# Kernel optimization log

Hardware: AMD Instinct MI355X
Metric: run time of the kernel (lower is better)

## Reference

```python
import jax, jax.numpy as jnp
import numpy as np

DIM = 1024
HEADS = 16
HIDDEN = 4 * DIM


def layernorm(x, g, b, eps=1e-5):
    mu = jnp.mean(x, axis=-1, keepdims=True)
    var = jnp.mean(jnp.square(x - mu), axis=-1, keepdims=True)
    return (x - mu) * jax.lax.rsqrt(var + eps) * g + b


def setup_inputs() -> dict:
    key = jax.random.key(0)
    ks = jax.random.split(key, 8)
    s = DIM ** -0.5
    return {
        "x": jax.random.normal(ks[0], (2, 2048, DIM), dtype=jnp.float32),
        "ln1_g": jnp.ones((DIM,), jnp.float32),
        "ln1_b": jnp.zeros((DIM,), jnp.float32),
        "qkv_w": jax.random.normal(ks[1], (DIM, 3 * DIM), jnp.float32) * s,
        "proj_w": jax.random.normal(ks[2], (DIM, DIM), jnp.float32) * s,
        "proj_b": jnp.zeros((DIM,), jnp.float32),
        "ln2_g": jnp.ones((DIM,), jnp.float32),
        "ln2_b": jnp.zeros((DIM,), jnp.float32),
        "fc1_w": jax.random.normal(ks[3], (DIM, HIDDEN), jnp.float32) * s,
        "fc1_b": jnp.zeros((HIDDEN,), jnp.float32),
        "fc2_w": jax.random.normal(ks[4], (HIDDEN, DIM), jnp.float32) * (HIDDEN ** -0.5),
        "fc2_b": jnp.zeros((DIM,), jnp.float32),
    }


def block_fwd(x, ln1_g, ln1_b, qkv_w, proj_w, proj_b, ln2_g, ln2_b,
              fc1_w, fc1_b, fc2_w, fc2_b):
    B, N, C = x.shape
    H = HEADS
    Dh = C // H
    scale = Dh ** -0.5
    # --- attention branch (pre-norm) ---
    h = layernorm(x, ln1_g, ln1_b)
    qkv = h @ qkv_w                     # [B,N,3C] (no bias: qkv_bias=False)
    qkv = qkv.reshape(B, N, 3, H, Dh)
    q = qkv[:, :, 0].transpose(0, 2, 1, 3)   # [B,H,N,Dh]
    k = qkv[:, :, 1].transpose(0, 2, 1, 3)
    v = qkv[:, :, 2].transpose(0, 2, 1, 3)
    attn = jnp.einsum('bhqd,bhkd->bhqk', q, k) * scale
    attn = jax.nn.softmax(attn, axis=-1)
    o = jnp.einsum('bhqk,bhkd->bhqd', attn, v)
    o = o.transpose(0, 2, 1, 3).reshape(B, N, C)
    x = x + (o @ proj_w + proj_b)
    # --- MLP branch (pre-norm) ---
    h = layernorm(x, ln2_g, ln2_b)
    h = jax.nn.gelu(h @ fc1_w + fc1_b, approximate=False)  # torch nn.GELU = exact erf
    x = x + (h @ fc2_w + fc2_b)
    return x


def reference(x, ln1_g, ln1_b, qkv_w, proj_w, proj_b, ln2_g, ln2_b,
              fc1_w, fc1_b, fc2_w, fc2_b):
    return block_fwd(x, ln1_g, ln1_b, qkv_w, proj_w, proj_b, ln2_g, ln2_b,
                     fc1_w, fc1_b, fc2_w, fc2_b)
```

## Files before the change

### kernel.cpp

```cpp
#include <hip/hip_runtime.h>
#include <math.h>

typedef unsigned short u16;
typedef unsigned int u32;
typedef __attribute__((ext_vector_type(8))) short short8;
typedef __attribute__((ext_vector_type(4))) float f32x4;
typedef __attribute__((ext_vector_type(2))) u32 u32x2;
typedef __attribute__((ext_vector_type(4))) u32 u32x4;
typedef __attribute__((ext_vector_type(4))) u16 u16x4;

typedef __attribute__((address_space(1))) const void gmem_t;
typedef __attribute__((address_space(3))) void lmem_t;

__device__ __forceinline__ u16 f2bf(float f) {
  u32 u = __builtin_bit_cast(u32, f);
  u = u + 0x7fffu + ((u >> 16) & 1u);
  return (u16)(u >> 16);
}

__device__ __forceinline__ u32 cvt_pk_bf16(float a, float b) {
  u32 r;
  asm("v_cvt_pk_bf16_f32 %0, %1, %2" : "=v"(r) : "v"(a), "v"(b));
  return r;
}

__device__ __forceinline__ void g2l16(const void* g, void* l) {
  __builtin_amdgcn_global_load_lds((gmem_t*)g, (lmem_t*)l, 16, 0, 0);
}

template <int N> __device__ __forceinline__ void waitcnt_vm() {
  if constexpr (N == 0)      asm volatile("s_waitcnt vmcnt(0)" ::: "memory");
  else if constexpr (N == 4) asm volatile("s_waitcnt vmcnt(4)" ::: "memory");
  else if constexpr (N == 6) asm volatile("s_waitcnt vmcnt(6)" ::: "memory");
  else if constexpr (N == 8) asm volatile("s_waitcnt vmcnt(8)" ::: "memory");
  else static_assert(N == 0 || N == 4 || N == 6 || N == 8, "add literal");
}

__global__ __launch_bounds__(256) void wtrans(const float* __restrict__ in,
                                              u16* __restrict__ out, int R, int C) {
  __shared__ float t[64][65];
  int tid = threadIdx.x;
  int nbx = C >> 6;
  int bx = blockIdx.x % nbx, by = blockIdx.x / nbx;
  int r0 = by << 6, c0 = bx << 6;
  int lr = tid >> 2, lc = (tid & 3) << 4;
  const float* src = in + (size_t)(r0 + lr) * C + c0 + lc;
#pragma unroll
  for (int j = 0; j < 4; ++j) {
    f32x4 v = *(const f32x4*)(src + j * 4);
    t[lr][lc + j * 4 + 0] = v.x; t[lr][lc + j * 4 + 1] = v.y;
    t[lr][lc + j * 4 + 2] = v.z; t[lr][lc + j * 4 + 3] = v.w;
  }
  __syncthreads();
  int oc = tid >> 2, orr = (tid & 3) << 4;
  u16* dst = out + (size_t)(c0 + oc) * R + r0 + orr;
  u32 u[8];
#pragma unroll
  for (int j = 0; j < 8; ++j)
    u[j] = (u32)f2bf(t[orr + 2 * j][oc]) | ((u32)f2bf(t[orr + 2 * j + 1][oc]) << 16);
  u32x4 v0; v0.x = u[0]; v0.y = u[1]; v0.z = u[2]; v0.w = u[3];
  u32x4 v1; v1.x = u[4]; v1.y = u[5]; v1.z = u[6]; v1.w = u[7];
  *(u32x4*)(dst) = v0;
  *(u32x4*)(dst + 8) = v1;
}

__global__ __launch_bounds__(256) void lnorm(const float* __restrict__ in,
                                             const float* __restrict__ gw,
                                             const float* __restrict__ bw,
                                             u16* __restrict__ out) {
  int r = blockIdx.x, tid = threadIdx.x;
  const f32x4 v = *((const f32x4*)(in + (size_t)r * 1024) + tid);
  float s = v.x + v.y + v.z + v.w;
  float ss = v.x * v.x + v.y * v.y + v.z * v.z + v.w * v.w;
#pragma unroll
  for (int o = 32; o >= 1; o >>= 1) { s += __shfl_xor(s, o); ss += __shfl_xor(ss, o); }
  __shared__ float red[8];
  int w = tid >> 6;
  if ((tid & 63) == 0) { red[w] = s; red[4 + w] = ss; }
  __syncthreads();
  s = red[0] + red[1] + red[2] + red[3];
  ss = red[4] + red[5] + red[6] + red[7];
  float mu = s * (1.0f / 1024.0f);
  float var = ss * (1.0f / 1024.0f) - mu * mu;
  float rstd = rsqrtf(var + 1e-5f);
  const f32x4 g4 = *((const f32x4*)gw + tid);
  const f32x4 b4 = *((const f32x4*)bw + tid);
  u16x4 o;
  o.x = f2bf((v.x - mu) * rstd * g4.x + b4.x);
  o.y = f2bf((v.y - mu) * rstd * g4.y + b4.y);
  o.z = f2bf((v.z - mu) * rstd * g4.z + b4.z);
  o.w = f2bf((v.w - mu) * rstd * g4.w + b4.w);
  *((u16x4*)(out + (size_t)r * 1024) + tid) = o;
}

template <int EPI, int BM, int BN>
__global__ __launch_bounds__(256, 2) void gemm_bt(
    const u16* __restrict__ A, const u16* __restrict__ BT, int M, int N, int K,
    const float* __restrict__ bias, const float* __restrict__ resid,
    float* __restrict__ fout, u16* __restrict__ bout,
    u16* __restrict__ bout2, u16* __restrict__ bout3) {
  constexpr int AIT = BM / 32, BIT = BN / 32;
  constexpr int L = AIT + BIT;
  constexpr int MR = BM / 32, NR = BN / 32;
  __shared__ __align__(16) u16 smA[2][BM * 64];
  __shared__ __align__(16) u16 smB[2][BN * 64];
  int tid = threadIdx.x;
  int w = tid >> 6, l = tid & 63, lq = l & 15, g = l >> 4;
  int nbx = N / BN;
  int t = (int)blockIdx.x;
  int cpx = (int)gridDim.x >> 3;
  t = (t & 7) * cpx + (t >> 3);
  int by = t / nbx, bx = t - by * nbx;
  long brow = (long)by * BM, bcol = (long)bx * BN;
  int wr = w >> 1, wc = w & 1;

  const u16* aS[AIT]; const u16* bS[BIT];
#pragma unroll
  for (int it = 0; it < AIT; ++it) {
    int p = it * 256 + tid;
    int row = p >> 3;
    int gc = (p & 7) ^ (row & 7);
    aS[it] = A + (size_t)(brow + row) * K + gc * 8;
  }
#pragma unroll
  for (int it = 0; it < BIT; ++it) {
    int p = it * 256 + tid;
    int row = p >> 3;
    int gc = (p & 7) ^ (row & 7);
    bS[it] = BT + (size_t)(bcol + row) * K + gc * 8;
  }
  auto STAGE = [&](int buf, int k0) {
#pragma unroll
    for (int it = 0; it < AIT; ++it) g2l16(aS[it] + k0, &smA[buf][it * 2048 + w * 512]);
#pragma unroll
    for (int it = 0; it < BIT; ++it) g2l16(bS[it] + k0, &smB[buf][it * 2048 + w * 512]);
  };

  f32x4 zero = {0.f, 0.f, 0.f, 0.f};
  f32x4 acc[MR][NR];
#pragma unroll
  for (int m = 0; m < MR; ++m)
#pragma unroll
    for (int n = 0; n < NR; ++n) acc[m][n] = zero;

  int NT = K >> 6;
  STAGE(0, 0);
  for (int tt = 0; tt < NT; ++tt) {
    int cur = tt & 1;
    int knext = ((tt + 1) == NT ? 0 : (tt + 1)) << 6;
    STAGE(cur ^ 1, knext);
    waitcnt_vm<L>();
    __builtin_amdgcn_s_barrier();
    asm volatile("" ::: "memory");

    const char* sA = (const char*)&smA[cur][0];
    const char* sB = (const char*)&smB[cur][0];
#pragma unroll
    for (int c = 0; c < 2; ++c) {
      short8 af[MR], bfb[NR];
#pragma unroll
      for (int m = 0; m < MR; ++m) {
        int r = wr * (BM / 2) + m * 16 + lq;
        af[m] = *(const short8*)(sA + r * 128 + ((g * 16 + c * 64) ^ ((r & 7) << 4)));
      }
#pragma unroll
      for (int n = 0; n < NR; ++n) {
        int r = wc * (BN / 2) + n * 16 + lq;
        bfb[n] = *(const short8*)(sB + r * 128 + ((g * 16 + c * 64) ^ ((r & 7) << 4)));
      }
#pragma unroll
      for (int m = 0; m < MR; ++m)
#pragma unroll
        for (int n = 0; n < NR; ++n)
          acc[m][n] = __builtin_amdgcn_mfma_f32_16x16x32_bf16(af[m], bfb[n], acc[m][n], 0, 0, 0);
    }
    asm volatile("" ::: "memory");
    __builtin_amdgcn_s_barrier();
  }
  waitcnt_vm<0>();

  long colbase = bcol + wc * (BN / 2);
#pragma unroll
  for (int m = 0; m < MR; ++m) {
#pragma unroll
    for (int n = 0; n < NR; ++n) {
      f32x4 v = acc[m][n];
      long col = colbase + n * 16 + lq;
      long row0 = brow + wr * (BM / 2) + m * 16 + g * 4;
      if constexpr (EPI == 0) {
        int part = (int)(bcol >> 10);
        long colq = col - ((long)part << 10);
        int hh = (int)(colq >> 6), d = (int)(colq & 63);
#pragma unroll
        for (int i = 0; i < 4; ++i) {
          long row = row0 + i;
          long b = row >> 11, nq = row & 2047;
          long bh = b * 16 + hh;
          u16 val = f2bf(v[i]);
          if (part == 0)      bout [(bh * 2048 + nq) * 64 + d] = val;
          else if (part == 1) bout2[(bh * 2048 + nq) * 64 + d] = val;
          else                bout3[(bh * 64 + d) * 2048 + nq] = val;
        }
      } else if constexpr (EPI == 1 || EPI == 3) {
        float bb = bias[col];
#pragma unroll
        for (int i = 0; i < 4; ++i) {
          long idx = (row0 + i) * N + col;
          fout[idx] = resid[idx] + v[i] + bb;
        }
      } else {
        float bb = bias[col];
#pragma unroll
        for (int i = 0; i < 4; ++i) {
          float xg = v[i] + bb;
          float ge = 0.5f * xg * (1.0f + erff(xg * 0.70710678118654752f));
          bout[(row0 + i) * N + col] = f2bf(ge);
        }
      }
    }
  }
}

__global__ __launch_bounds__(256, 2) void attn_fwd(const u16* __restrict__ qb,
                                                   const u16* __restrict__ kb,
                                                   const u16* __restrict__ vtb,
                                                   u16* __restrict__ ob) {
  __shared__ __align__(16) u16 kl[2][64 * 64];
  __shared__ __align__(16) u16 vl[2][64 * 64];
  __shared__ __align__(16) u16 pl[4][32 * 72];
  int tid = threadIdx.x;
  int w = tid >> 6, l = tid & 63, lq = l & 15, g = l >> 4;
  int bh = (int)blockIdx.x & 31;
  int qt = (int)blockIdx.x >> 5;

  const u16* qr = qb + ((size_t)bh * 2048 + qt * 128 + w * 32 + lq) * 64 + g * 8;
  short8 qA0 = *(const short8*)qr;
  short8 qA1 = *(const short8*)(qr + 32);
  short8 qB0 = *(const short8*)(qr + 16 * 64);
  short8 qB1 = *(const short8*)(qr + 16 * 64 + 32);

  const u16* kS[2]; const u16* vS[2];
#pragma unroll
  for (int it = 0; it < 2; ++it) {
    int p = it * 256 + tid;
    int row = p >> 3;
    int gc = (p & 7) ^ (row & 7);
    kS[it] = kb + ((size_t)bh * 2048 + row) * 64 + gc * 8;
    vS[it] = vtb + ((size_t)bh * 64 + row) * 2048 + gc * 8;
  }
  auto issue = [&](int buf, int kt0) {
#pragma unroll
    for (int it = 0; it < 2; ++it) {
      g2l16(kS[it] + (size_t)kt0 * 64, &kl[buf][it * 2048 + w * 512]);
      g2l16(vS[it] + kt0,              &vl[buf][it * 2048 + w * 512]);
    }
  };

  f32x4 zero = {0.f, 0.f, 0.f, 0.f};
  f32x4 accO0[4] = {zero, zero, zero, zero};
  f32x4 accO1[4] = {zero, zero, zero, zero};
  f32x4 accl0 = zero, accl1 = zero;
  const float sc = 0.125f * 1.44269504088896f;
  u32x4 ov; ov.x = ov.y = ov.z = ov.w = 0x3F803F80u;
  short8 onesf = __builtin_bit_cast(short8, ov);

  issue(0, 0);
  for (int t = 0; t < 32; ++t) {
    int cur = t & 1;
    issue(cur ^ 1, ((t + 1) & 31) << 6);
    waitcnt_vm<4>();
    __builtin_amdgcn_s_barrier();
    asm volatile("" ::: "memory");

    const char* klc = (const char*)&kl[cur][0];
    const char* vlc = (const char*)&vl[cur][0];

    f32x4 s0[4], s1[4];
#pragma unroll
    for (int kt = 0; kt < 4; ++kt) {
      int r = kt * 16 + lq;
      short8 a0 = *(const short8*)(klc + (r * 128 + ((g * 16) ^ ((r & 7) << 4))));
      short8 a1 = *(const short8*)(klc + (r * 128 + ((g * 16 + 64) ^ ((r & 7) << 4))));
      s0[kt] = __builtin_amdgcn_mfma_f32_16x16x32_bf16(a0, qA0, zero, 0, 0, 0);
      s0[kt] = __builtin_amdgcn_mfma_f32_16x16x32_bf16(a1, qA1, s0[kt], 0, 0, 0);
      s1[kt] = __builtin_amdgcn_mfma_f32_16x16x32_bf16(a0, qB0, zero, 0, 0, 0);
      s1[kt] = __builtin_amdgcn_mfma_f32_16x16x32_bf16(a1, qB1, s1[kt], 0, 0, 0);
    }

    char* plw = (char*)&pl[w][0];
#pragma unroll
    for (int kt = 0; kt < 4; ++kt) {
      u32x2 uA, uB;
      uA.x = cvt_pk_bf16(exp2f(s0[kt][0] * sc - 12.0f), exp2f(s0[kt][1] * sc - 12.0f));
      uA.y = cvt_pk_bf16(exp2f(s0[kt][2] * sc - 12.0f), exp2f(s0[kt][3] * sc - 12.0f));
      uB.x = cvt_pk_bf16(exp2f(s1[kt][0] * sc - 12.0f), exp2f(s1[kt][1] * sc - 12.0f));
      uB.y = cvt_pk_bf16(exp2f(s1[kt][2] * sc - 12.0f), exp2f(s1[kt][3] * sc - 12.0f));
      *(u32x2*)(plw + lq * 144 + kt * 32 + g * 8) = uA;
      *(u32x2*)(plw + 2304 + lq * 144 + kt * 32 + g * 8) = uB;
    }

#pragma unroll
    for (int c = 0; c < 2; ++c) {
      short8 paA = *(const short8*)(plw + lq * 144 + g * 16 + c * 64);
      short8 paB = *(const short8*)(plw + 2304 + lq * 144 + g * 16 + c * 64);
#pragma unroll
      for (int dt = 0; dt < 4; ++dt) {
        int r = dt * 16 + lq;
        short8 b = *(const short8*)(vlc + (r * 128 + ((g * 16 + c * 64) ^ ((r & 7) << 4))));
        accO0[dt] = __builtin_amdgcn_mfma_f32_16x16x32_bf16(paA, b, accO0[dt], 0, 0, 0);
        accO1[dt] = __builtin_amdgcn_mfma_f32_16x16x32_bf16(paB, b, accO1[dt], 0, 0, 0);
      }
      accl0 = __builtin_amdgcn_mfma_f32_16x16x32_bf16(paA, onesf, accl0, 0, 0, 0);
      accl1 = __builtin_amdgcn_mfma_f32_16x16x32_bf16(paB, onesf, accl1, 0, 0, 0);
    }
    asm volatile("" ::: "memory");
    __builtin_amdgcn_s_barrier();
  }
  waitcnt_vm<0>();

  float li0[4], li1[4];
#pragma unroll
  for (int i = 0; i < 4; ++i) { li0[i] = 1.0f / accl0[i]; li1[i] = 1.0f / accl1[i]; }
  int b = bh >> 4, h = bh & 15;
  long qbase = (long)qt * 128 + w * 32 + g * 4;
#pragma unroll
  for (int dt = 0; dt < 4; ++dt)
#pragma unroll
    for (int i = 0; i < 4; ++i) {
      long d = dt * 16 + lq;
      ob[((long)b * 2048 + qbase + i) * 1024 + h * 64 + d]      = f2bf(accO0[dt][i] * li0[i]);
      ob[((long)b * 2048 + qbase + 16 + i) * 1024 + h * 64 + d] = f2bf(accO1[dt][i] * li1[i]);
    }
}

extern "C" void kernel_launch(void* const* d_in, const int* in_sizes, int n_in,
                              void* d_out, int out_size, void* d_ws, size_t ws_size,
                              hipStream_t stream) {
  const float* x     = (const float*)d_in[0];
  const float* ln1g  = (const float*)d_in[1];
  const float* ln1b  = (const float*)d_in[2];
  const float* qkvw  = (const float*)d_in[3];
  const float* projw = (const float*)d_in[4];
  const float* projb = (const float*)d_in[5];
  const float* ln2g  = (const float*)d_in[6];
  const float* ln2b  = (const float*)d_in[7];
  const float* fc1w  = (const float*)d_in[8];
  const float* fc1b  = (const float*)d_in[9];
  const float* fc2w  = (const float*)d_in[10];
  const float* fc2b  = (const float*)d_in[11];
  char* ws = (char*)d_ws;
  u16* qkv_wt  = (u16*)(ws + 0);
  u16* proj_wt = (u16*)(ws + 6291456);
  u16* fc1_wt  = (u16*)(ws + 8388608);
  u16* fc2_wt  = (u16*)(ws + 16777216);
  u16* h       = (u16*)(ws + 25165824);
  u16* qbuf    = (u16*)(ws + 33554432);
  u16* kbuf    = (u16*)(ws + 41943040);
  u16* vtbuf   = (u16*)(ws + 50331648);
  u16* aout    = (u16*)(ws + 58720256);
  float* y1    = (float*)(ws + 67108864);
  u16* gbuf    = (u16*)(ws + 33554432);
  float* outp  = (float*)d_out;

  wtrans<<<768, 256, 0, stream>>>(qkvw, qkv_wt, 1024, 3072);
  wtrans<<<256, 256, 0, stream>>>(projw, proj_wt, 1024, 1024);
  wtrans<<<1024, 256, 0, stream>>>(fc1w, fc1_wt, 1024, 4096);
  wtrans<<<1024, 256, 0, stream>>>(fc2w, fc2_wt, 4096, 1024);

  lnorm<<<4096, 256, 0, stream>>>(x, ln1g, ln1b, h);
  gemm_bt<0, 128, 128><<<768, 256, 0, stream>>>(h, qkv_wt, 4096, 3072, 1024,
                                      nullptr, nullptr, nullptr, qbuf, kbuf, vtbuf);
  attn_fwd<<<512, 256, 0, stream>>>(qbuf, kbuf, vtbuf, aout);
  gemm_bt<1, 64, 128><<<512, 256, 0, stream>>>(aout, proj_wt, 4096, 1024, 1024,
                                      projb, x, y1, nullptr, nullptr, nullptr);
  lnorm<<<4096, 256, 0, stream>>>(y1, ln2g, ln2b, h);
  gemm_bt<2, 128, 128><<<1024, 256, 0, stream>>>(h, fc1_wt, 4096, 4096, 1024,
                                       fc1b, nullptr, nullptr, gbuf, nullptr, nullptr);
  gemm_bt<3, 64, 128><<<512, 256, 0, stream>>>(gbuf, fc2_wt, 4096, 1024, 4096,
                                      fc2b, y1, outp, nullptr, nullptr, nullptr);
}
```

Before: 280.2 us.

## Halve attention query tile per block, raise occupancy, merge weight transposes

Each attention wave now handles 16 query rows instead of 32. This doubles the grid to 1024 blocks, shrinks the per-wave P staging buffer to an XOR-swizzled 16x64 layout, and raises launch bounds to 4 blocks per CU. K/V fragment loads are hoisted ahead of the MFMA groups, which are wrapped in s_setprio to favour matrix issue. The four weight-transpose launches are merged into one kernel that dispatches on block index. The trade-off is that each K/V tile fetched into LDS is reused across half as many queries, roughly doubling K/V global traffic in exchange for more latency hiding.

Result: faster. 271.1 us (-3.2%).

```diff
diff --git a/kernel.cpp b/kernel.cpp
--- a/kernel.cpp
+++ b/kernel.cpp
@@ -36,12 +36,21 @@
   else static_assert(N == 0 || N == 4 || N == 6 || N == 8, "add literal");
 }
 
-__global__ __launch_bounds__(256) void wtrans(const float* __restrict__ in,
-                                              u16* __restrict__ out, int R, int C) {
+__global__ __launch_bounds__(256) void wtrans_all(
+    const float* __restrict__ qkvw, const float* __restrict__ projw,
+    const float* __restrict__ fc1w, const float* __restrict__ fc2w,
+    u16* __restrict__ o_qkv, u16* __restrict__ o_proj,
+    u16* __restrict__ o_fc1, u16* __restrict__ o_fc2) {
+  int id = (int)blockIdx.x;
+  const float* in; u16* out; int R, C, bid;
+  if (id < 768)       { in = qkvw;  out = o_qkv;  R = 1024; C = 3072; bid = id; }
+  else if (id < 1024) { in = projw; out = o_proj; R = 1024; C = 1024; bid = id - 768; }
+  else if (id < 2048) { in = fc1w;  out = o_fc1;  R = 1024; C = 4096; bid = id - 1024; }
+  else                { in = fc2w;  out = o_fc2;  R = 4096; C = 1024; bid = id - 2048; }
   __shared__ float t[64][65];
   int tid = threadIdx.x;
   int nbx = C >> 6;
-  int bx = blockIdx.x % nbx, by = blockIdx.x / nbx;
+  int bx = bid % nbx, by = bid / nbx;
   int r0 = by << 6, c0 = bx << 6;
   int lr = tid >> 2, lc = (tid & 3) << 4;
   const float* src = in + (size_t)(r0 + lr) * C + c0 + lc;
@@ -221,23 +230,21 @@
   }
 }
 
-__global__ __launch_bounds__(256, 2) void attn_fwd(const u16* __restrict__ qb,
+__global__ __launch_bounds__(256, 4) void attn_fwd(const u16* __restrict__ qb,
                                                    const u16* __restrict__ kb,
                                                    const u16* __restrict__ vtb,
                                                    u16* __restrict__ ob) {
   __shared__ __align__(16) u16 kl[2][64 * 64];
   __shared__ __align__(16) u16 vl[2][64 * 64];
-  __shared__ __align__(16) u16 pl[4][32 * 72];
+  __shared__ __align__(16) u16 pl[4][16 * 64];
   int tid = threadIdx.x;
   int w = tid >> 6, l = tid & 63, lq = l & 15, g = l >> 4;
   int bh = (int)blockIdx.x & 31;
   int qt = (int)blockIdx.x >> 5;
 
-  const u16* qr = qb + ((size_t)bh * 2048 + qt * 128 + w * 32 + lq) * 64 + g * 8;
-  short8 qA0 = *(const short8*)qr;
-  short8 qA1 = *(const short8*)(qr + 32);
-  short8 qB0 = *(const short8*)(qr + 16 * 64);
-  short8 qB1 = *(const short8*)(qr + 16 * 64 + 32);
+  const u16* qr = qb + ((size_t)bh * 2048 + qt * 64 + w * 16 + lq) * 64 + g * 8;
+  short8 qf0 = *(const short8*)qr;
+  short8 qf1 = *(const short8*)(qr + 32);
 
   const u16* kS[2]; const u16* vS[2];
 #pragma unroll
@@ -257,12 +264,12 @@
   };
 
   f32x4 zero = {0.f, 0.f, 0.f, 0.f};
-  f32x4 accO0[4] = {zero, zero, zero, zero};
-  f32x4 accO1[4] = {zero, zero, zero, zero};
-  f32x4 accl0 = zero, accl1 = zero;
+  f32x4 accO[4] = {zero, zero, zero, zero};
+  f32x4 accl = zero;
   const float sc = 0.125f * 1.44269504088896f;
   u32x4 ov; ov.x = ov.y = ov.z = ov.w = 0x3F803F80u;
   short8 onesf = __builtin_bit_cast(short8, ov);
+  int plswz = (lq & 7) << 4;
 
   issue(0, 0);
   for (int t = 0; t < 32; ++t) {
@@ -275,61 +282,63 @@
     const char* klc = (const char*)&kl[cur][0];
     const char* vlc = (const char*)&vl[cur][0];
 
-    f32x4 s0[4], s1[4];
+    f32x4 s[4];
+    short8 ka0[4], ka1[4];
 #pragma unroll
     for (int kt = 0; kt < 4; ++kt) {
       int r = kt * 16 + lq;
-      short8 a0 = *(const short8*)(klc + (r * 128 + ((g * 16) ^ ((r & 7) << 4))));
-      short8 a1 = *(const short8*)(klc + (r * 128 + ((g * 16 + 64) ^ ((r & 7) << 4))));
-      s0[kt] = __builtin_amdgcn_mfma_f32_16x16x32_bf16(a0, qA0, zero, 0, 0, 0);
-      s0[kt] = __builtin_amdgcn_mfma_f32_16x16x32_bf16(a1, qA1, s0[kt], 0, 0, 0);
-      s1[kt] = __builtin_amdgcn_mfma_f32_16x16x32_bf16(a0, qB0, zero, 0, 0, 0);
-      s1[kt] = __builtin_amdgcn_mfma_f32_16x16x32_bf16(a1, qB1, s1[kt], 0, 0, 0);
-    }
+      ka0[kt] = *(const short8*)(klc + (r * 128 + ((g * 16) ^ ((r & 7) << 4))));
+      ka1[kt] = *(const short8*)(klc + (r * 128 + ((g * 16 + 64) ^ ((r & 7) << 4))));
+    }
+    __builtin_amdgcn_s_setprio(1);
+#pragma unroll
+    for (int kt = 0; kt < 4; ++kt) {
+      s[kt] = __builtin_amdgcn_mfma_f32_16x16x32_bf16(ka0[kt], qf0, zero, 0, 0, 0);
+      s[kt] = __builtin_amdgcn_mfma_f32_16x16x32_bf16(ka1[kt], qf1, s[kt], 0, 0, 0);
+    }
+    __builtin_amdgcn_s_setprio(0);
 
     char* plw = (char*)&pl[w][0];
 #pragma unroll
     for (int kt = 0; kt < 4; ++kt) {
-      u32x2 uA, uB;
-      uA.x = cvt_pk_bf16(exp2f(s0[kt][0] * sc - 12.0f), exp2f(s0[kt][1] * sc - 12.0f));
-      uA.y = cvt_pk_bf16(exp2f(s0[kt][2] * sc - 12.0f), exp2f(s0[kt][3] * sc - 12.0f));
-      uB.x = cvt_pk_bf16(exp2f(s1[kt][0] * sc - 12.0f), exp2f(s1[kt][1] * sc - 12.0f));
-      uB.y = cvt_pk_bf16(exp2f(s1[kt][2] * sc - 12.0f), exp2f(s1[kt][3] * sc - 12.0f));
-      *(u32x2*)(plw + lq * 144 + kt * 32 + g * 8) = uA;
-      *(u32x2*)(plw + 2304 + lq * 144 + kt * 32 + g * 8) = uB;
+      u32x2 uu;
+      uu.x = cvt_pk_bf16(exp2f(s[kt][0] * sc - 12.0f), exp2f(s[kt][1] * sc - 12.0f));
+      uu.y = cvt_pk_bf16(exp2f(s[kt][2] * sc - 12.0f), exp2f(s[kt][3] * sc - 12.0f));
+      *(u32x2*)(plw + ((lq * 128 + kt * 32 + g * 8) ^ plswz)) = uu;
     }
 
 #pragma unroll
     for (int c = 0; c < 2; ++c) {
-      short8 paA = *(const short8*)(plw + lq * 144 + g * 16 + c * 64);
-      short8 paB = *(const short8*)(plw + 2304 + lq * 144 + g * 16 + c * 64);
+      short8 pa = *(const short8*)(plw + ((lq * 128 + g * 16 + c * 64) ^ plswz));
+      short8 vf[4];
 #pragma unroll
       for (int dt = 0; dt < 4; ++dt) {
         int r = dt * 16 + lq;
-        short8 b = *(const short8*)(vlc + (r * 128 + ((g * 16 + c * 64) ^ ((r & 7) << 4))));
-        accO0[dt] = __builtin_amdgcn_mfma_f32_16x16x32_bf16(paA, b, accO0[dt], 0, 0, 0);
-        accO1[dt] = __builtin_amdgcn_mfma_f32_16x16x32_bf16(paB, b, accO1[dt], 0, 0, 0);
+        vf[dt] = *(const short8*)(vlc + (r * 128 + ((g * 16 + c * 64) ^ ((r & 7) << 4))));
       }
-      accl0 = __builtin_amdgcn_mfma_f32_16x16x32_bf16(paA, onesf, accl0, 0, 0, 0);
-      accl1 = __builtin_amdgcn_mfma_f32_16x16x32_bf16(paB, onesf, accl1, 0, 0, 0);
+      __builtin_amdgcn_s_setprio(1);
+#pragma unroll
+      for (int dt = 0; dt < 4; ++dt)
+        accO[dt] = __builtin_amdgcn_mfma_f32_16x16x32_bf16(pa, vf[dt], accO[dt], 0, 0, 0);
+      accl = __builtin_amdgcn_mfma_f32_16x16x32_bf16(pa, onesf, accl, 0, 0, 0);
+      __builtin_amdgcn_s_setprio(0);
     }
     asm volatile("" ::: "memory");
     __builtin_amdgcn_s_barrier();
   }
   waitcnt_vm<0>();
 
-  float li0[4], li1[4];
-#pragma unroll
-  for (int i = 0; i < 4; ++i) { li0[i] = 1.0f / accl0[i]; li1[i] = 1.0f / accl1[i]; }
+  float li[4];
+#pragma unroll
+  for (int i = 0; i < 4; ++i) li[i] = 1.0f / accl[i];
   int b = bh >> 4, h = bh & 15;
-  long qbase = (long)qt * 128 + w * 32 + g * 4;
+  long qbase = (long)qt * 64 + w * 16 + g * 4;
 #pragma unroll
   for (int dt = 0; dt < 4; ++dt)
 #pragma unroll
     for (int i = 0; i < 4; ++i) {
       long d = dt * 16 + lq;
-      ob[((long)b * 2048 + qbase + i) * 1024 + h * 64 + d]      = f2bf(accO0[dt][i] * li0[i]);
-      ob[((long)b * 2048 + qbase + 16 + i) * 1024 + h * 64 + d] = f2bf(accO1[dt][i] * li1[i]);
+      ob[((long)b * 2048 + qbase + i) * 1024 + h * 64 + d] = f2bf(accO[dt][i] * li[i]);
     }
 }
 
@@ -362,15 +371,13 @@
   u16* gbuf    = (u16*)(ws + 33554432);
   float* outp  = (float*)d_out;
 
-  wtrans<<<768, 256, 0, stream>>>(qkvw, qkv_wt, 1024, 3072);
-  wtrans<<<256, 256, 0, stream>>>(projw, proj_wt, 1024, 1024);
-  wtrans<<<1024, 256, 0, stream>>>(fc1w, fc1_wt, 1024, 4096);
-  wtrans<<<1024, 256, 0, stream>>>(fc2w, fc2_wt, 4096, 1024);
+  wtrans_all<<<3072, 256, 0, stream>>>(qkvw, projw, fc1w, fc2w,
+                                       qkv_wt, proj_wt, fc1_wt, fc2_wt);
 
   lnorm<<<4096, 256, 0, stream>>>(x, ln1g, ln1b, h);
   gemm_bt<0, 128, 128><<<768, 256, 0, stream>>>(h, qkv_wt, 4096, 3072, 1024,
                                       nullptr, nullptr, nullptr, qbuf, kbuf, vtbuf);
-  attn_fwd<<<512, 256, 0, stream>>>(qbuf, kbuf, vtbuf, aout);
+  attn_fwd<<<1024, 256, 0, stream>>>(qbuf, kbuf, vtbuf, aout);
   gemm_bt<1, 64, 128><<<512, 256, 0, stream>>>(aout, proj_wt, 4096, 1024, 1024,
                                       projb, x, y1, nullptr, nullptr, nullptr);
   lnorm<<<4096, 256, 0, stream>>>(y1, ln2g, ln2b, h);
```
